# Kernel optimization log

Measured on AMD Instinct MI355X. Metric: run time of the kernel, lower is better.

The kernel has to match this reference:

```python
import jax, jax.numpy as jnp
import numpy as np

HIDDEN = 768

def setup_inputs() -> dict:
    key = jax.random.key(0)
    ks = jax.random.split(key, 7)
    x = jax.random.normal(ks[0], (4, 4096, HIDDEN), dtype=jnp.float32)
    s = 1.0 / np.sqrt(HIDDEN)
    Wq = jax.random.uniform(ks[1], (HIDDEN, HIDDEN), minval=-s, maxval=s, dtype=jnp.float32)
    Wk = jax.random.uniform(ks[2], (HIDDEN, HIDDEN), minval=-s, maxval=s, dtype=jnp.float32)
    Wv = jax.random.uniform(ks[3], (HIDDEN, HIDDEN), minval=-s, maxval=s, dtype=jnp.float32)
    bq = jax.random.uniform(ks[4], (HIDDEN,), minval=-s, maxval=s, dtype=jnp.float32)
    bk = jax.random.uniform(ks[5], (HIDDEN,), minval=-s, maxval=s, dtype=jnp.float32)
    bv = jax.random.uniform(ks[6], (HIDDEN,), minval=-s, maxval=s, dtype=jnp.float32)
    return {"x": x, "Wq": Wq, "bq": bq, "Wk": Wk, "bk": bk, "Wv": Wv, "bv": bv}

def reference(x, Wq, bq, Wk, bk, Wv, bv):
    # q,k,v: [b, s, d]
    q = jnp.einsum('bsd,de->bse', x, Wq.T) + bq
    k = jnp.einsum('bsd,de->bse', x, Wk.T) + bk
    v = jnp.einsum('bsd,de->bse', x, Wv.T) + bv
    scale = 1.0 / jnp.sqrt(jnp.asarray(x.shape[-1], dtype=x.dtype))
    scores = jnp.einsum('bqd,bkd->bqk', q, k) * scale  # [b, s, s]
    attn = jax.nn.softmax(scores, axis=-1)
    return jnp.einsum('bqk,bkd->bqd', attn, v)
```

## Files before the change

kernel.cpp:

```cpp
#include <hip/hip_runtime.h>
#include <stdint.h>

typedef unsigned short u16;
typedef __attribute__((ext_vector_type(8))) short    bf16x8;
typedef __attribute__((ext_vector_type(4))) float    f32x4;

__device__ __forceinline__ u16 f2bf(float f) {
    unsigned u = __float_as_uint(f);
    u = (u + 0x7fffu + ((u >> 16) & 1u)) >> 16;
    return (u16)u;
}
__device__ __forceinline__ void gload16(const u16* g, u16* l) {
    __builtin_amdgcn_global_load_lds((const __attribute__((address_space(1))) void*)g,
                                     (__attribute__((address_space(3))) void*)l,
                                     16, 0, 0);
}

__global__ __launch_bounds__(256) void cast_bf16_kernel(const float* __restrict__ in,
                                                        u16* __restrict__ out, int n4) {
    int i = blockIdx.x * 256 + threadIdx.x;
    if (i < n4) {
        float4 f = ((const float4*)in)[i];
        ushort4 o;
        o.x = f2bf(f.x); o.y = f2bf(f.y); o.z = f2bf(f.z); o.w = f2bf(f.w);
        ((ushort4*)out)[i] = o;
    }
}

__global__ __launch_bounds__(256) void cast3_bf16_kernel(const float* __restrict__ w0,
                                                         const float* __restrict__ w1,
                                                         const float* __restrict__ w2,
                                                         u16* __restrict__ out) {
    const float* src = (blockIdx.y == 0) ? w0 : (blockIdx.y == 1) ? w1 : w2;
    int i = blockIdx.x * 256 + threadIdx.x;
    float4 f = ((const float4*)src)[i];
    ushort4 o;
    o.x = f2bf(f.x); o.y = f2bf(f.y); o.z = f2bf(f.z); o.w = f2bf(f.w);
    ((ushort4*)out)[(size_t)blockIdx.y * 147456 + i] = o;
}

__global__ __launch_bounds__(256) void transpose_bf16_kernel(const u16* __restrict__ V,
                                                             u16* __restrict__ Vt,
                                                             float* __restrict__ rsum) {
    __shared__ u16 tile[32][33];
    const int t = threadIdx.x;
    if (blockIdx.x == 0 && blockIdx.z == 0) {
        int idx = blockIdx.y * 256 + t;
        if (idx < 16384) rsum[idx] = 0.f;
    }
    const size_t z = blockIdx.z;
    const u16* Vb  = V  + z * (size_t)4096 * 2304;
    u16*       Vtb = Vt + z * (size_t)768 * 4096;
    const int c0 = blockIdx.x * 32;
    const int r0 = blockIdx.y * 32;
    const int lr = t >> 3;
    const int lc = (t & 7) * 4;
    ushort4 in = *(const ushort4*)&Vb[(size_t)(r0 + lr) * 2304 + c0 + lc];
    tile[lr][lc + 0] = in.x; tile[lr][lc + 1] = in.y;
    tile[lr][lc + 2] = in.z; tile[lr][lc + 3] = in.w;
    __syncthreads();
    ushort4 o;
    o.x = tile[lc + 0][lr]; o.y = tile[lc + 1][lr];
    o.z = tile[lc + 2][lr]; o.w = tile[lc + 3][lr];
    *(ushort4*)&Vtb[(size_t)(c0 + lr) * 4096 + r0 + lc] = o;
}

template <int EPI, int SWIZ>
__global__ __launch_bounds__(256) void gemm_bt_kernel(
        const u16* __restrict__ A, const u16* __restrict__ B, void* __restrict__ Cv,
        const float* __restrict__ b0, const float* __restrict__ b1, const float* __restrict__ b2,
        float* __restrict__ rs, float scale, int K,
        int lda, int ldb, int ldc, long batchA, long batchB, long batchC) {
    __shared__ __align__(16) u16 As[128 * 32];
    __shared__ __align__(16) u16 Bs[128 * 32];

    int bx, by, bz;
    if (SWIZ) {
        const int lin = blockIdx.x;
        const int c = lin & 7, p = lin >> 3;
        bx = p % 6;
        const int strip = 16 * c + p / 6;
        by = strip & 31; bz = strip >> 5;
    } else {
        bx = blockIdx.x; by = blockIdx.y; bz = blockIdx.z;
    }

    const int t = threadIdx.x;
    const long z = bz;
    const u16* Ab = A + z * batchA + (long)by * 128 * lda;
    const u16* Bb = B + z * batchB + (long)bx * 128 * ldb;

    const int lane = t & 63;
    const int wave = t >> 6;
    const int wm = wave >> 1, wn = wave & 1;
    const int quad = lane >> 4;
    const int frow = lane & 15;

    f32x4 acc[4][4];
#pragma unroll
    for (int i = 0; i < 4; i++)
#pragma unroll
        for (int j = 0; j < 4; j++)
#pragma unroll
            for (int e = 0; e < 4; e++) acc[i][j][e] = 0.f;

    const int c0 = t, c1 = t + 256;
    const int ar0 = c0 >> 2, as0 = (c0 & 3) * 8;
    const int ar1 = c1 >> 2, as1 = (c1 & 3) * 8;

    for (int kt = 0; kt < K; kt += 32) {
        gload16(Ab + (long)ar0 * lda + kt + as0, &As[c0 * 8]);
        gload16(Ab + (long)ar1 * lda + kt + as1, &As[c1 * 8]);
        gload16(Bb + (long)ar0 * ldb + kt + as0, &Bs[c0 * 8]);
        gload16(Bb + (long)ar1 * ldb + kt + as1, &Bs[c1 * 8]);
        __syncthreads();

        bf16x8 af[4], bfr[4];
#pragma unroll
        for (int i = 0; i < 4; i++) {
            af[i]  = *(const bf16x8*)&As[(wm * 64 + i * 16 + frow) * 32 + quad * 8];
            bfr[i] = *(const bf16x8*)&Bs[(wn * 64 + i * 16 + frow) * 32 + quad * 8];
        }
#pragma unroll
        for (int i = 0; i < 4; i++)
#pragma unroll
            for (int j = 0; j < 4; j++)
                acc[i][j] = __builtin_amdgcn_mfma_f32_16x16x32_bf16(af[i], bfr[j], acc[i][j], 0, 0, 0);
        __syncthreads();
    }

    const int m_base = by * 128 + wm * 64;
    const int n_base = bx * 128 + wn * 64;

    float rowpart[4][4];
    if (EPI == 1) {
#pragma unroll
        for (int i = 0; i < 4; i++)
#pragma unroll
            for (int r = 0; r < 4; r++) rowpart[i][r] = 0.f;
    }

#pragma unroll
    for (int i = 0; i < 4; i++) {
#pragma unroll
        for (int j = 0; j < 4; j++) {
            const int col  = n_base + j * 16 + frow;
            const int row0 = m_base + i * 16 + quad * 4;
            if (EPI == 0) {
                const int seg = n_base / 768;
                const float* bp = ((seg == 0) ? b0 : (seg == 1) ? b1 : b2) - (long)seg * 768;
                const float bb = bp[col];
                u16* C = (u16*)Cv + z * batchC;
#pragma unroll
                for (int r = 0; r < 4; r++)
                    C[(long)(row0 + r) * ldc + col] = f2bf(acc[i][j][r] + bb);
            } else if (EPI == 1) {
                u16* C = (u16*)Cv + z * batchC;
#pragma unroll
                for (int r = 0; r < 4; r++) {
                    float e = __expf(acc[i][j][r] * scale);
                    C[(long)(row0 + r) * ldc + col] = f2bf(e);
                    rowpart[i][r] += e;
                }
            } else {
                float* C = (float*)Cv + z * batchC;
#pragma unroll
                for (int r = 0; r < 4; r++) {
                    const float inv = 1.0f / rs[z * 4096 + row0 + r];
                    C[(long)(row0 + r) * ldc + col] = acc[i][j][r] * inv;
                }
            }
        }
    }

    if (EPI == 1) {
#pragma unroll
        for (int i = 0; i < 4; i++)
#pragma unroll
            for (int r = 0; r < 4; r++) {
                float v = rowpart[i][r];
                v += __shfl_xor(v, 1); v += __shfl_xor(v, 2);
                v += __shfl_xor(v, 4); v += __shfl_xor(v, 8);
                if (frow == 0)
                    atomicAdd(&rs[z * 4096 + m_base + i * 16 + quad * 4 + r], v);
            }
    }
}

extern "C" void kernel_launch(void* const* d_in, const int* in_sizes, int n_in,
                              void* d_out, int out_size, void* d_ws, size_t ws_size,
                              hipStream_t stream) {
    const float* x  = (const float*)d_in[0];
    const float* Wq = (const float*)d_in[1];
    const float* bq = (const float*)d_in[2];
    const float* Wk = (const float*)d_in[3];
    const float* bk = (const float*)d_in[4];
    const float* Wv = (const float*)d_in[5];
    const float* bv = (const float*)d_in[6];
    float* out = (float*)d_out;

    uint8_t* ws = (uint8_t*)d_ws;
    u16*   xb   = (u16*)(ws + 0);
    u16*   Vt   = (u16*)(ws + 0);
    u16*   QKV  = (u16*)(ws + 25165824);
    u16*   E    = (u16*)(ws + 100663296);
    u16*   Wqkv = (u16*)(ws + 234881024);
    float* rsum = (float*)(ws + 234881024);

    cast_bf16_kernel<<<12288, 256, 0, stream>>>(x, xb, 3145728);
    cast3_bf16_kernel<<<dim3(576, 3), 256, 0, stream>>>(Wq, Wk, Wv, Wqkv);

    gemm_bt_kernel<0, 0><<<dim3(18, 128, 1), 256, 0, stream>>>(
        xb, Wqkv, QKV, bq, bk, bv, nullptr, 1.f, 768, 768, 768, 2304, 0, 0, 0);

    transpose_bf16_kernel<<<dim3(24, 128, 4), 256, 0, stream>>>(QKV + 1536, Vt, rsum);

    gemm_bt_kernel<1, 0><<<dim3(32, 32, 4), 256, 0, stream>>>(
        QKV, QKV + 768, E, nullptr, nullptr, nullptr, rsum, 0.036084391824351615f,
        768, 2304, 2304, 4096, (long)4096 * 2304, (long)4096 * 2304, (long)4096 * 4096);

    gemm_bt_kernel<2, 1><<<768, 256, 0, stream>>>(
        E, Vt, out, nullptr, nullptr, nullptr, rsum, 1.f,
        4096, 4096, 4096, 768, (long)4096 * 4096, (long)768 * 4096, (long)4096 * 768);
}
```

Before: 504.4 us.

## Generalize XCD-aware block swizzle to all GEMMs and tighten register use

```diff
diff --git a/kernel.cpp b/kernel.cpp
--- a/kernel.cpp
+++ b/kernel.cpp
@@ -65,25 +65,22 @@
     *(ushort4*)&Vtb[(size_t)(c0 + lr) * 4096 + r0 + lc] = o;
 }
 
-template <int EPI, int SWIZ>
-__global__ __launch_bounds__(256) void gemm_bt_kernel(
+template <int EPI, int NBX, int NGRID, int NBY>
+__global__ __launch_bounds__(256, 4) void gemm_bt_kernel(
         const u16* __restrict__ A, const u16* __restrict__ B, void* __restrict__ Cv,
         const float* __restrict__ b0, const float* __restrict__ b1, const float* __restrict__ b2,
-        float* __restrict__ rs, float scale, int K,
+        float* __restrict__ rs, float s2, int K,
         int lda, int ldb, int ldc, long batchA, long batchB, long batchC) {
     __shared__ __align__(16) u16 As[128 * 32];
     __shared__ __align__(16) u16 Bs[128 * 32];
 
-    int bx, by, bz;
-    if (SWIZ) {
-        const int lin = blockIdx.x;
-        const int c = lin & 7, p = lin >> 3;
-        bx = p % 6;
-        const int strip = 16 * c + p / 6;
-        by = strip & 31; bz = strip >> 5;
-    } else {
-        bx = blockIdx.x; by = blockIdx.y; bz = blockIdx.z;
-    }
+    constexpr int SPX = NGRID / (8 * NBX);
+    const int lin = blockIdx.x;
+    const int c = lin & 7, p = lin >> 3;
+    const int bx = p % NBX;
+    const int strip = c * SPX + p / NBX;
+    const int by = strip % NBY;
+    const int bz = strip / NBY;
 
     const int t = threadIdx.x;
     const long z = bz;
@@ -115,65 +112,60 @@
         gload16(Bb + (long)ar1 * ldb + kt + as1, &Bs[c1 * 8]);
         __syncthreads();
 
-        bf16x8 af[4], bfr[4];
+        bf16x8 bfr[4];
+#pragma unroll
+        for (int j = 0; j < 4; j++)
+            bfr[j] = *(const bf16x8*)&Bs[(wn * 64 + j * 16 + frow) * 32 + quad * 8];
 #pragma unroll
         for (int i = 0; i < 4; i++) {
-            af[i]  = *(const bf16x8*)&As[(wm * 64 + i * 16 + frow) * 32 + quad * 8];
-            bfr[i] = *(const bf16x8*)&Bs[(wn * 64 + i * 16 + frow) * 32 + quad * 8];
-        }
-#pragma unroll
-        for (int i = 0; i < 4; i++)
+            bf16x8 af = *(const bf16x8*)&As[(wm * 64 + i * 16 + frow) * 32 + quad * 8];
 #pragma unroll
             for (int j = 0; j < 4; j++)
-                acc[i][j] = __builtin_amdgcn_mfma_f32_16x16x32_bf16(af[i], bfr[j], acc[i][j], 0, 0, 0);
+                acc[i][j] = __builtin_amdgcn_mfma_f32_16x16x32_bf16(af, bfr[j], acc[i][j], 0, 0, 0);
+        }
         __syncthreads();
     }
 
     const int m_base = by * 128 + wm * 64;
     const int n_base = bx * 128 + wn * 64;
 
-    float rowpart[4][4];
-    if (EPI == 1) {
-#pragma unroll
-        for (int i = 0; i < 4; i++)
-#pragma unroll
-            for (int r = 0; r < 4; r++) rowpart[i][r] = 0.f;
-    }
-
-#pragma unroll
-    for (int i = 0; i < 4; i++) {
+    if (EPI == 0) {
+        const int seg = n_base / 768;
+        const float* bp = (seg == 0) ? b0 : (seg == 1) ? b1 : b2;
+        u16* C = (u16*)Cv + z * batchC;
 #pragma unroll
         for (int j = 0; j < 4; j++) {
-            const int col  = n_base + j * 16 + frow;
-            const int row0 = m_base + i * 16 + quad * 4;
-            if (EPI == 0) {
-                const int seg = n_base / 768;
-                const float* bp = ((seg == 0) ? b0 : (seg == 1) ? b1 : b2) - (long)seg * 768;
-                const float bb = bp[col];
-                u16* C = (u16*)Cv + z * batchC;
+            const int col = n_base + j * 16 + frow;
+            const float bb = bp[col - seg * 768];
+#pragma unroll
+            for (int i = 0; i < 4; i++) {
+                const int row0 = m_base + i * 16 + quad * 4;
 #pragma unroll
                 for (int r = 0; r < 4; r++)
                     C[(long)(row0 + r) * ldc + col] = f2bf(acc[i][j][r] + bb);
-            } else if (EPI == 1) {
-                u16* C = (u16*)Cv + z * batchC;
+            }
+        }
+    } else if (EPI == 1) {
+        u16* C = (u16*)Cv + z * batchC;
+        float rowpart[4][4];
+#pragma unroll
+        for (int i = 0; i < 4; i++)
+#pragma unroll
+            for (int r = 0; r < 4; r++) rowpart[i][r] = 0.f;
+#pragma unroll
+        for (int i = 0; i < 4; i++) {
+            const int row0 = m_base + i * 16 + quad * 4;
+#pragma unroll
+            for (int j = 0; j < 4; j++) {
+                const int col = n_base + j * 16 + frow;
 #pragma unroll
                 for (int r = 0; r < 4; r++) {
-                    float e = __expf(acc[i][j][r] * scale);
+                    float e = exp2f(acc[i][j][r] * s2);
                     C[(long)(row0 + r) * ldc + col] = f2bf(e);
                     rowpart[i][r] += e;
                 }
-            } else {
-                float* C = (float*)Cv + z * batchC;
-#pragma unroll
-                for (int r = 0; r < 4; r++) {
-                    const float inv = 1.0f / rs[z * 4096 + row0 + r];
-                    C[(long)(row0 + r) * ldc + col] = acc[i][j][r] * inv;
-                }
-            }
-        }
-    }
-
-    if (EPI == 1) {
+            }
+        }
 #pragma unroll
         for (int i = 0; i < 4; i++)
 #pragma unroll
@@ -184,6 +176,22 @@
                 if (frow == 0)
                     atomicAdd(&rs[z * 4096 + m_base + i * 16 + quad * 4 + r], v);
             }
+    } else {
+        float* C = (float*)Cv + z * batchC;
+#pragma unroll
+        for (int i = 0; i < 4; i++) {
+            const int row0 = m_base + i * 16 + quad * 4;
+            float inv[4];
+#pragma unroll
+            for (int r = 0; r < 4; r++) inv[r] = 1.0f / rs[z * 4096 + row0 + r];
+#pragma unroll
+            for (int j = 0; j < 4; j++) {
+                const int col = n_base + j * 16 + frow;
+#pragma unroll
+                for (int r = 0; r < 4; r++)
+                    C[(long)(row0 + r) * ldc + col] = acc[i][j][r] * inv[r];
+            }
+        }
     }
 }
 
@@ -210,16 +218,16 @@
     cast_bf16_kernel<<<12288, 256, 0, stream>>>(x, xb, 3145728);
     cast3_bf16_kernel<<<dim3(576, 3), 256, 0, stream>>>(Wq, Wk, Wv, Wqkv);
 
-    gemm_bt_kernel<0, 0><<<dim3(18, 128, 1), 256, 0, stream>>>(
-        xb, Wqkv, QKV, bq, bk, bv, nullptr, 1.f, 768, 768, 768, 2304, 0, 0, 0);
+    gemm_bt_kernel<0, 18, 2304, 128><<<2304, 256, 0, stream>>>(
+        xb, Wqkv, QKV, bq, bk, bv, nullptr, 0.f, 768, 768, 768, 2304, 0, 0, 0);
 
     transpose_bf16_kernel<<<dim3(24, 128, 4), 256, 0, stream>>>(QKV + 1536, Vt, rsum);
 
-    gemm_bt_kernel<1, 0><<<dim3(32, 32, 4), 256, 0, stream>>>(
-        QKV, QKV + 768, E, nullptr, nullptr, nullptr, rsum, 0.036084391824351615f,
+    gemm_bt_kernel<1, 32, 4096, 32><<<4096, 256, 0, stream>>>(
+        QKV, QKV + 768, E, nullptr, nullptr, nullptr, rsum, 0.05205954822032348f,
         768, 2304, 2304, 4096, (long)4096 * 2304, (long)4096 * 2304, (long)4096 * 4096);
 
-    gemm_bt_kernel<2, 1><<<768, 256, 0, stream>>>(
-        E, Vt, out, nullptr, nullptr, nullptr, rsum, 1.f,
+    gemm_bt_kernel<2, 6, 768, 32><<<768, 256, 0, stream>>>(
+        E, Vt, out, nullptr, nullptr, nullptr, rsum, 0.f,
         4096, 4096, 4096, 768, (long)4096 * 4096, (long)768 * 4096, (long)4096 * 768);
 }
```

New measurement: 484.9 us. 1.04x faster.
